# Kernel tuning notes

Measured on AMD Instinct MI355X. Metric: run time of the kernel, lower is better.

The kernel has to match this reference:

```python
import jax, jax.numpy as jnp
import numpy as np

NUM_EMBEDDINGS = 1024
EMBEDDING_DIM = 64
COMMITMENT_COST = 0.25
EPS = 1e-12  # F.normalize clamp eps


def _l2_normalize(v):
    n = jnp.linalg.norm(v, axis=-1, keepdims=True)
    return v / jnp.maximum(n, EPS)


def setup_inputs() -> dict:
    key = jax.random.key(0)
    k_x, k_w = jax.random.split(key)
    x = jax.random.normal(k_x, (262144, EMBEDDING_DIM), dtype=jnp.float32)
    # nn.init.uniform_(weight, -1/K, 1/K)
    lim = 1.0 / NUM_EMBEDDINGS
    codebook = jax.random.uniform(k_w, (NUM_EMBEDDINGS, EMBEDDING_DIM),
                                  minval=-lim, maxval=lim, dtype=jnp.float32)
    return {"x": x, "codebook": codebook}


def reference(x, codebook):
    # Normalized vectors used only for nearest-neighbor search.
    xn = _l2_normalize(x)                      # [N, D]
    cn = _l2_normalize(codebook)               # [K, D]
    # ||xn||^2 + ||cn||^2 - 2 xn.cn  -> [N, K]
    distances = (jnp.sum(xn * xn, axis=1, keepdims=True)
                 + jnp.sum(cn * cn, axis=1)
                 - 2.0 * jnp.einsum('nd,kd->nk', xn, cn))
    encoding_indices = jnp.argmin(distances, axis=1)           # [N]
    quantized_unnormalized = codebook[encoding_indices]        # [N, D]
    sg = jax.lax.stop_gradient
    codebook_loss = jnp.mean((quantized_unnormalized - sg(x)) ** 2)
    commitment_loss = jnp.mean((x - sg(quantized_unnormalized)) ** 2)
    quantized_ste = x + sg(quantized_unnormalized - x)
    return quantized_ste, codebook_loss, commitment_loss, encoding_indices
```

## Files before the change

### kernel.cpp

```cpp
#include <hip/hip_runtime.h>
#include <math.h>

#define EPS 1e-12f
constexpr int N_ROWS = 262144;
constexpr int KCODES = 1024;
constexpr int DIM    = 64;
constexpr int CAP    = 65536;
constexpr int CHUNK_SH = 16384;

typedef __attribute__((ext_vector_type(8)))  short  short8;
typedef __attribute__((ext_vector_type(16))) float  float16;

__device__ inline unsigned short f2bf(float f) {
    unsigned int u = __float_as_uint(f);
    u = u + 0x7fff + ((u >> 16) & 1);
    return (unsigned short)(u >> 16);
}
__device__ inline float bf2f(unsigned short s) {
    return __uint_as_float(((unsigned int)s) << 16);
}

__global__ __launch_bounds__(64)
void vq_prep(const float* __restrict__ cb, float* __restrict__ cnT,
             float* __restrict__ cc, unsigned short* __restrict__ frag,
             int* __restrict__ cnt, float* __restrict__ dloss) {
    int n = blockIdx.x;
    int d = threadIdx.x;
    float v = cb[n * DIM + d];
    float s = v * v;
    #pragma unroll
    for (int off = 32; off; off >>= 1) s += __shfl_xor(s, off, 64);
    float vn = v / fmaxf(sqrtf(s), EPS);
    cnT[d * KCODES + n] = vn;
    float s2 = vn * vn;
    #pragma unroll
    for (int off = 32; off; off >>= 1) s2 += __shfl_xor(s2, off, 64);
    if (d == 0) cc[n] = s2;
    unsigned short hi = f2bf(vn);
    unsigned short lo = f2bf(vn - bf2f(hi));
    int c = n >> 7, t = (n >> 5) & 3;
    int lane = (n & 31) + 32 * ((d >> 3) & 1);
    int si = d >> 4, j = d & 7;
    size_t base = (size_t)(((c * 4 + t) * 4 + si) * 2) * 512 + lane * 8 + j;
    frag[base]       = hi;
    frag[base + 512] = lo;
    if (n == 0 && d == 0) { *cnt = 0; *dloss = 0.f; }
}

__global__ __launch_bounds__(256, 2)
void vq_mfma(const float* __restrict__ x, const unsigned short* __restrict__ frag,
             const float* __restrict__ cb, float* __restrict__ out_q,
             float* __restrict__ out_idx, int* __restrict__ cnt,
             int* __restrict__ list, float* __restrict__ partial) {
    __shared__ unsigned short Blds[2][CHUNK_SH];
    __shared__ int   ridx[256];
    __shared__ float redl[4];

    const int tid = threadIdx.x;
    const int w = tid >> 6, l = tid & 63;
    const int lc = l & 31, h = l >> 5;
    const int row0 = blockIdx.x * 256;

    short8 ahi[2][4], alo[2][4];
    #pragma unroll
    for (int tile = 0; tile < 2; ++tile) {
        int row = row0 + w * 64 + tile * 32 + lc;
        float xv[4][8]; float ss = 0.f;
        #pragma unroll
        for (int s = 0; s < 4; ++s) {
            const float* p = x + (size_t)row * DIM + s * 16 + h * 8;
            float4 a = *(const float4*)p;
            float4 b = *(const float4*)(p + 4);
            xv[s][0]=a.x; xv[s][1]=a.y; xv[s][2]=a.z; xv[s][3]=a.w;
            xv[s][4]=b.x; xv[s][5]=b.y; xv[s][6]=b.z; xv[s][7]=b.w;
            ss += a.x*a.x + a.y*a.y + a.z*a.z + a.w*a.w
                + b.x*b.x + b.y*b.y + b.z*b.z + b.w*b.w;
        }
        ss += __shfl_xor(ss, 32, 64);
        float inv = 1.0f / fmaxf(sqrtf(ss), EPS);
        #pragma unroll
        for (int s = 0; s < 4; ++s)
            #pragma unroll
            for (int j = 0; j < 8; ++j) {
                float v = xv[s][j] * inv;
                unsigned short hb = f2bf(v);
                unsigned short lb = f2bf(v - bf2f(hb));
                ahi[tile][s][j] = (short)hb;
                alo[tile][s][j] = (short)lb;
            }
    }

    int m1[2][16], m2[2][16];
    #pragma unroll
    for (int tile = 0; tile < 2; ++tile)
        #pragma unroll
        for (int r = 0; r < 16; ++r) { m1[tile][r] = 0; m2[tile][r] = 0; }

    {
        const unsigned short* g = frag + (w * 8) * 512 + l * 8;
        #pragma unroll
        for (int q = 0; q < 8; ++q)
            __builtin_amdgcn_global_load_lds(
                (const __attribute__((address_space(1))) unsigned int*)(g + q * 512),
                (__attribute__((address_space(3))) unsigned int*)&Blds[0][(w * 8 + q) * 512],
                16, 0, 0);
    }

    for (int c = 0; c < 8; ++c) {
        __syncthreads();
        if (c < 7) {
            const unsigned short* g = frag + (size_t)(c + 1) * CHUNK_SH + (w * 8) * 512 + l * 8;
            #pragma unroll
            for (int q = 0; q < 8; ++q)
                __builtin_amdgcn_global_load_lds(
                    (const __attribute__((address_space(1))) unsigned int*)(g + q * 512),
                    (__attribute__((address_space(3))) unsigned int*)&Blds[(c + 1) & 1][(w * 8 + q) * 512],
                    16, 0, 0);
        }
        const unsigned short* B = Blds[c & 1];
        #pragma unroll
        for (int t = 0; t < 4; ++t) {
            short8 bhi[4], blo[4];
            #pragma unroll
            for (int s = 0; s < 4; ++s) {
                bhi[s] = *((const short8*)&B[((t * 4 + s) * 2    ) * 512] + l);
                blo[s] = *((const short8*)&B[((t * 4 + s) * 2 + 1) * 512] + l);
            }
            int vcode = (1023 - c * 128 - t * 32) - lc;
            #pragma unroll
            for (int tile = 0; tile < 2; ++tile) {
                float16 acc;
                #pragma unroll
                for (int r = 0; r < 16; ++r) acc[r] = 2.0f;
                #pragma unroll
                for (int s = 0; s < 4; ++s) {
                    acc = __builtin_amdgcn_mfma_f32_32x32x16_bf16(ahi[tile][s], bhi[s], acc, 0, 0, 0);
                    acc = __builtin_amdgcn_mfma_f32_32x32x16_bf16(alo[tile][s], bhi[s], acc, 0, 0, 0);
                    acc = __builtin_amdgcn_mfma_f32_32x32x16_bf16(ahi[tile][s], blo[s], acc, 0, 0, 0);
                }
                #pragma unroll
                for (int r = 0; r < 16; ++r) {
                    int k = (__float_as_int(acc[r]) & (int)0xFFFFFC00) | vcode;
                    int t0 = min(m1[tile][r], k);
                    m1[tile][r] = max(m1[tile][r], k);
                    m2[tile][r] = max(m2[tile][r], t0);
                }
            }
        }
    }

    #pragma unroll
    for (int tile = 0; tile < 2; ++tile)
        #pragma unroll
        for (int r = 0; r < 16; ++r) {
            int a = m1[tile][r], b = m2[tile][r];
            #pragma unroll
            for (int off = 1; off < 32; off <<= 1) {
                int oa = __shfl_xor(a, off, 64);
                int ob = __shfl_xor(b, off, 64);
                int nb = max(max(b, ob), min(a, oa));
                a = max(a, oa); b = nb;
            }
            if (lc == 0) {
                int rowl = w * 64 + tile * 32 + (r & 3) + 8 * (r >> 2) + 4 * h;
                ridx[rowl] = 1023 - (a & 1023);
                if (((a >> 10) - (b >> 10)) <= 1) {
                    int p = atomicAdd(cnt, 1);
                    if (p < CAP) list[p] = row0 + rowl;
                }
            }
        }
    __syncthreads();

    out_idx[row0 + tid] = (float)ridx[tid];

    float lsum = 0.f;
    const float4* cb4 = (const float4*)cb;
    const float4* x4  = (const float4*)x;
    float4*       o4  = (float4*)out_q;
    #pragma unroll
    for (int i = 0; i < 16; ++i) {
        int f = tid + 256 * i;
        int r = f >> 4, c4 = f & 15;
        float4 q  = cb4[ridx[r] * 16 + c4];
        float4 xr = x4[(size_t)row0 * 16 + f];
        o4[(size_t)row0 * 16 + f] = q;
        float dx = q.x - xr.x, dy = q.y - xr.y, dz = q.z - xr.z, dw = q.w - xr.w;
        lsum += dx * dx + dy * dy + dz * dz + dw * dw;
    }
    #pragma unroll
    for (int off = 32; off; off >>= 1) lsum += __shfl_xor(lsum, off, 64);
    if (l == 0) redl[w] = lsum;
    __syncthreads();
    if (tid == 0) partial[blockIdx.x] = redl[0] + redl[1] + redl[2] + redl[3];
}

__global__ __launch_bounds__(256)
void vq_recheck(const float* __restrict__ x, const float* __restrict__ cnT,
                const float* __restrict__ cc, const float* __restrict__ cb,
                const int* __restrict__ cnt, const int* __restrict__ list,
                float* __restrict__ out_idx, float* __restrict__ out_q,
                float* __restrict__ dloss) {
    int w = threadIdx.x >> 6, l = threadIdx.x & 63;
    int wid = blockIdx.x * 4 + w, nw = gridDim.x * 4;
    int n = *cnt; if (n > CAP) n = CAP;
    for (int e = wid; e < n; e += nw) {
        int row = list[e];
        float xl = x[(size_t)row * DIM + l];
        float ss = xl * xl;
        #pragma unroll
        for (int off = 32; off; off >>= 1) ss += __shfl_xor(ss, off, 64);
        float inv = 1.0f / fmaxf(sqrtf(ss), EPS);
        float dot[16];
        #pragma unroll
        for (int kk = 0; kk < 16; ++kk) dot[kk] = 0.f;
        for (int d = 0; d < 64; ++d) {
            float xd = __shfl(xl, d, 64);
            #pragma unroll
            for (int kk = 0; kk < 16; ++kk)
                dot[kk] = fmaf(xd, cnT[d * KCODES + l + 64 * kk], dot[kk]);
        }
        float best = INFINITY; int bix = 0x7fffffff;
        #pragma unroll
        for (int kk = 0; kk < 16; ++kk) {
            int k = l + 64 * kk;
            float dist = cc[k] - 2.0f * (inv * dot[kk]);
            if (dist < best) { best = dist; bix = k; }
        }
        #pragma unroll
        for (int off = 1; off < 64; off <<= 1) {
            float ob = __shfl_xor(best, off, 64);
            int   oi = __shfl_xor(bix,  off, 64);
            if (ob < best || (ob == best && oi < bix)) { best = ob; bix = oi; }
        }
        int oldi = (int)out_idx[row];
        if (bix != oldi) {
            float qn = cb[(size_t)bix  * DIM + l];
            float qo = cb[(size_t)oldi * DIM + l];
            float an = qn - xl, ao = qo - xl;
            float dl = an * an - ao * ao;
            #pragma unroll
            for (int off = 32; off; off >>= 1) dl += __shfl_xor(dl, off, 64);
            out_q[(size_t)row * DIM + l] = qn;
            if (l == 0) { out_idx[row] = (float)bix; atomicAdd(dloss, dl); }
        }
    }
}

__global__ __launch_bounds__(256)
void vq_final(const float* __restrict__ partial, const float* __restrict__ dloss,
              float* __restrict__ out_loss) {
    float s = 0.f;
    for (int i = threadIdx.x; i < 1024; i += 256) s += partial[i];
    #pragma unroll
    for (int off = 32; off; off >>= 1) s += __shfl_xor(s, off, 64);
    __shared__ float red[4];
    if ((threadIdx.x & 63) == 0) red[threadIdx.x >> 6] = s;
    __syncthreads();
    if (threadIdx.x == 0) {
        float t = red[0] + red[1] + red[2] + red[3] + *dloss;
        float m = t / (float)((size_t)N_ROWS * DIM);
        out_loss[0] = m;
        out_loss[1] = m;
    }
}

extern "C" void kernel_launch(void* const* d_in, const int* in_sizes, int n_in,
                              void* d_out, int out_size, void* d_ws, size_t ws_size,
                              hipStream_t stream) {
    const float* x  = (const float*)d_in[0];
    const float* cb = (const float*)d_in[1];
    float* out = (float*)d_out;
    float* out_q    = out;
    float* out_loss = out + (size_t)N_ROWS * DIM;
    float* out_idx  = out_loss + 2;

    char* ws = (char*)d_ws;
    float*          cnT     = (float*)(ws);
    float*          cc      = (float*)(ws + 262144);
    unsigned short* frag    = (unsigned short*)(ws + 266240);
    int*            cnt     = (int*)(ws + 528384);
    float*          dloss   = (float*)(ws + 528388);
    int*            list    = (int*)(ws + 528400);
    float*          partial = (float*)(ws + 790544);

    vq_prep   <<<KCODES, 64, 0, stream>>>(cb, cnT, cc, frag, cnt, dloss);
    vq_mfma   <<<N_ROWS / 256, 256, 0, stream>>>(x, frag, cb, out_q, out_idx, cnt, list, partial);
    vq_recheck<<<512, 256, 0, stream>>>(x, cnT, cc, cb, cnt, list, out_idx, out_q, dloss);
    vq_final  <<<1, 256, 0, stream>>>(partial, dloss, out_loss);
}
```

Measured before the change: 240.3 us.

## Halve rows per block and codebook chunk to raise occupancy, batch recheck atomics

The main MFMA kernel now processes 128 rows per block with one 32-row tile per wave instead of two, halving A-fragment and min-tracking registers and raising the launch-bounds occupancy target from 2 to 4 blocks. The codebook LDS chunk is halved to 64 codes, with the prep kernel's fragment layout changed to match and 16 pipeline iterations instead of 8. Near-tie rows flagged for the exact recheck are now collected per wave with one batched atomicAdd instead of one atomic per row. The cost is that each codebook B fragment read from LDS is reused by one tile instead of two, more blocks load the full codebook, and there are twice as many partial sums.

New measurement: 246.4 us. 1.03x slower.

```diff
diff --git a/kernel.cpp b/kernel.cpp
--- a/kernel.cpp
+++ b/kernel.cpp
@@ -6,7 +6,7 @@
 constexpr int KCODES = 1024;
 constexpr int DIM    = 64;
 constexpr int CAP    = 65536;
-constexpr int CHUNK_SH = 16384;
+constexpr int CHUNK_SH = 8192;
 
 typedef __attribute__((ext_vector_type(8)))  short  short8;
 typedef __attribute__((ext_vector_type(16))) float  float16;
@@ -20,12 +20,12 @@
     return __uint_as_float(((unsigned int)s) << 16);
 }
 
-__global__ __launch_bounds__(64)
+__global__ __launch_bounds__(256)
 void vq_prep(const float* __restrict__ cb, float* __restrict__ cnT,
              float* __restrict__ cc, unsigned short* __restrict__ frag,
              int* __restrict__ cnt, float* __restrict__ dloss) {
-    int n = blockIdx.x;
-    int d = threadIdx.x;
+    int n = blockIdx.x * 4 + (threadIdx.x >> 6);
+    int d = threadIdx.x & 63;
     float v = cb[n * DIM + d];
     float s = v * v;
     #pragma unroll
@@ -38,33 +38,32 @@
     if (d == 0) cc[n] = s2;
     unsigned short hi = f2bf(vn);
     unsigned short lo = f2bf(vn - bf2f(hi));
-    int c = n >> 7, t = (n >> 5) & 3;
+    int c = n >> 6, t = (n >> 5) & 1;
     int lane = (n & 31) + 32 * ((d >> 3) & 1);
     int si = d >> 4, j = d & 7;
-    size_t base = (size_t)(((c * 4 + t) * 4 + si) * 2) * 512 + lane * 8 + j;
+    size_t base = (size_t)c * CHUNK_SH + (size_t)((t * 4 + si) * 2) * 512 + lane * 8 + j;
     frag[base]       = hi;
     frag[base + 512] = lo;
     if (n == 0 && d == 0) { *cnt = 0; *dloss = 0.f; }
 }
 
-__global__ __launch_bounds__(256, 2)
+__global__ __launch_bounds__(256, 4)
 void vq_mfma(const float* __restrict__ x, const unsigned short* __restrict__ frag,
              const float* __restrict__ cb, float* __restrict__ out_q,
              float* __restrict__ out_idx, int* __restrict__ cnt,
              int* __restrict__ list, float* __restrict__ partial) {
     __shared__ unsigned short Blds[2][CHUNK_SH];
-    __shared__ int   ridx[256];
+    __shared__ int   ridx[128];
     __shared__ float redl[4];
 
     const int tid = threadIdx.x;
     const int w = tid >> 6, l = tid & 63;
     const int lc = l & 31, h = l >> 5;
-    const int row0 = blockIdx.x * 256;
-
-    short8 ahi[2][4], alo[2][4];
-    #pragma unroll
-    for (int tile = 0; tile < 2; ++tile) {
-        int row = row0 + w * 64 + tile * 32 + lc;
+    const int row0 = blockIdx.x * 128;
+    const int row  = row0 + w * 32 + lc;
+
+    short8 ahi[4], alo[4];
+    {
         float xv[4][8]; float ss = 0.f;
         #pragma unroll
         for (int s = 0; s < 4; ++s) {
@@ -85,101 +84,107 @@
                 float v = xv[s][j] * inv;
                 unsigned short hb = f2bf(v);
                 unsigned short lb = f2bf(v - bf2f(hb));
-                ahi[tile][s][j] = (short)hb;
-                alo[tile][s][j] = (short)lb;
-            }
-    }
-
-    int m1[2][16], m2[2][16];
-    #pragma unroll
-    for (int tile = 0; tile < 2; ++tile)
-        #pragma unroll
-        for (int r = 0; r < 16; ++r) { m1[tile][r] = 0; m2[tile][r] = 0; }
+                ahi[s][j] = (short)hb;
+                alo[s][j] = (short)lb;
+            }
+    }
+
+    int m1[16], m2[16];
+    #pragma unroll
+    for (int r = 0; r < 16; ++r) { m1[r] = 0; m2[r] = 0; }
 
     {
-        const unsigned short* g = frag + (w * 8) * 512 + l * 8;
-        #pragma unroll
-        for (int q = 0; q < 8; ++q)
+        const unsigned short* g = frag + tid * 8;
+        #pragma unroll
+        for (int q = 0; q < 4; ++q)
             __builtin_amdgcn_global_load_lds(
-                (const __attribute__((address_space(1))) unsigned int*)(g + q * 512),
-                (__attribute__((address_space(3))) unsigned int*)&Blds[0][(w * 8 + q) * 512],
+                (const __attribute__((address_space(1))) unsigned int*)(g + q * 2048),
+                (__attribute__((address_space(3))) unsigned int*)&Blds[0][(tid + 256 * q) * 8],
                 16, 0, 0);
     }
 
-    for (int c = 0; c < 8; ++c) {
+    for (int c = 0; c < 16; ++c) {
         __syncthreads();
-        if (c < 7) {
-            const unsigned short* g = frag + (size_t)(c + 1) * CHUNK_SH + (w * 8) * 512 + l * 8;
-            #pragma unroll
-            for (int q = 0; q < 8; ++q)
+        if (c < 15) {
+            const unsigned short* g = frag + (size_t)(c + 1) * CHUNK_SH + tid * 8;
+            #pragma unroll
+            for (int q = 0; q < 4; ++q)
                 __builtin_amdgcn_global_load_lds(
-                    (const __attribute__((address_space(1))) unsigned int*)(g + q * 512),
-                    (__attribute__((address_space(3))) unsigned int*)&Blds[(c + 1) & 1][(w * 8 + q) * 512],
+                    (const __attribute__((address_space(1))) unsigned int*)(g + q * 2048),
+                    (__attribute__((address_space(3))) unsigned int*)&Blds[(c + 1) & 1][(tid + 256 * q) * 8],
                     16, 0, 0);
         }
         const unsigned short* B = Blds[c & 1];
         #pragma unroll
-        for (int t = 0; t < 4; ++t) {
-            short8 bhi[4], blo[4];
+        for (int t = 0; t < 2; ++t) {
+            float16 acc;
+            #pragma unroll
+            for (int r = 0; r < 16; ++r) acc[r] = 2.0f;
             #pragma unroll
             for (int s = 0; s < 4; ++s) {
-                bhi[s] = *((const short8*)&B[((t * 4 + s) * 2    ) * 512] + l);
-                blo[s] = *((const short8*)&B[((t * 4 + s) * 2 + 1) * 512] + l);
-            }
-            int vcode = (1023 - c * 128 - t * 32) - lc;
-            #pragma unroll
-            for (int tile = 0; tile < 2; ++tile) {
-                float16 acc;
-                #pragma unroll
-                for (int r = 0; r < 16; ++r) acc[r] = 2.0f;
-                #pragma unroll
-                for (int s = 0; s < 4; ++s) {
-                    acc = __builtin_amdgcn_mfma_f32_32x32x16_bf16(ahi[tile][s], bhi[s], acc, 0, 0, 0);
-                    acc = __builtin_amdgcn_mfma_f32_32x32x16_bf16(alo[tile][s], bhi[s], acc, 0, 0, 0);
-                    acc = __builtin_amdgcn_mfma_f32_32x32x16_bf16(ahi[tile][s], blo[s], acc, 0, 0, 0);
-                }
-                #pragma unroll
-                for (int r = 0; r < 16; ++r) {
-                    int k = (__float_as_int(acc[r]) & (int)0xFFFFFC00) | vcode;
-                    int t0 = min(m1[tile][r], k);
-                    m1[tile][r] = max(m1[tile][r], k);
-                    m2[tile][r] = max(m2[tile][r], t0);
-                }
-            }
-        }
-    }
-
-    #pragma unroll
-    for (int tile = 0; tile < 2; ++tile)
-        #pragma unroll
-        for (int r = 0; r < 16; ++r) {
-            int a = m1[tile][r], b = m2[tile][r];
-            #pragma unroll
-            for (int off = 1; off < 32; off <<= 1) {
-                int oa = __shfl_xor(a, off, 64);
-                int ob = __shfl_xor(b, off, 64);
-                int nb = max(max(b, ob), min(a, oa));
-                a = max(a, oa); b = nb;
-            }
-            if (lc == 0) {
-                int rowl = w * 64 + tile * 32 + (r & 3) + 8 * (r >> 2) + 4 * h;
-                ridx[rowl] = 1023 - (a & 1023);
-                if (((a >> 10) - (b >> 10)) <= 1) {
-                    int p = atomicAdd(cnt, 1);
-                    if (p < CAP) list[p] = row0 + rowl;
-                }
-            }
-        }
+                short8 bhi = *((const short8*)&B[((t * 4 + s) * 2    ) * 512] + l);
+                short8 blo = *((const short8*)&B[((t * 4 + s) * 2 + 1) * 512] + l);
+                acc = __builtin_amdgcn_mfma_f32_32x32x16_bf16(ahi[s], bhi, acc, 0, 0, 0);
+                acc = __builtin_amdgcn_mfma_f32_32x32x16_bf16(alo[s], bhi, acc, 0, 0, 0);
+                acc = __builtin_amdgcn_mfma_f32_32x32x16_bf16(ahi[s], blo, acc, 0, 0, 0);
+            }
+            int vcode = (1023 - c * 64 - t * 32) - lc;
+            #pragma unroll
+            for (int r = 0; r < 16; ++r) {
+                int k = (__float_as_int(acc[r]) & (int)0xFFFFFC00) | vcode;
+                int t0 = min(m1[r], k);
+                m1[r] = max(m1[r], k);
+                m2[r] = max(m2[r], t0);
+            }
+        }
+    }
+
+    int flags = 0;
+    #pragma unroll
+    for (int r = 0; r < 16; ++r) {
+        int a = m1[r], b = m2[r];
+        #pragma unroll
+        for (int off = 1; off < 32; off <<= 1) {
+            int oa = __shfl_xor(a, off, 64);
+            int ob = __shfl_xor(b, off, 64);
+            int nb = max(max(b, ob), min(a, oa));
+            a = max(a, oa); b = nb;
+        }
+        if (lc == 0) {
+            int rr = (r & 3) + 8 * (r >> 2) + 4 * h;
+            ridx[w * 32 + rr] = 1023 - (a & 1023);
+            if (((a >> 10) - (b >> 10)) <= 1) flags |= (1 << r);
+        }
+    }
+
+    {
+        int f0 = __shfl(flags, 0, 64), fh = __shfl(flags, 32, 64);
+        int tot = __popc(f0) + __popc(fh);
+        int base = 0;
+        if (l == 0 && tot) base = atomicAdd(cnt, tot);
+        base = __shfl(base, 0, 64);
+        if (tot && (l == 0 || l == 32)) {
+            int off = (l == 32) ? __popc(f0) : 0;
+            int fl = flags;
+            while (fl) {
+                int r = __ffs(fl) - 1; fl &= fl - 1;
+                int rr = (r & 3) + 8 * (r >> 2) + 4 * h;
+                int p = base + off;
+                if (p < CAP) list[p] = row0 + w * 32 + rr;
+                ++off;
+            }
+        }
+    }
     __syncthreads();
 
-    out_idx[row0 + tid] = (float)ridx[tid];
+    if (tid < 128) out_idx[row0 + tid] = (float)ridx[tid];
 
     float lsum = 0.f;
     const float4* cb4 = (const float4*)cb;
     const float4* x4  = (const float4*)x;
     float4*       o4  = (float4*)out_q;
     #pragma unroll
-    for (int i = 0; i < 16; ++i) {
+    for (int i = 0; i < 8; ++i) {
         int f = tid + 256 * i;
         int r = f >> 4, c4 = f & 15;
         float4 q  = cb4[ridx[r] * 16 + c4];
@@ -251,7 +256,7 @@
 void vq_final(const float* __restrict__ partial, const float* __restrict__ dloss,
               float* __restrict__ out_loss) {
     float s = 0.f;
-    for (int i = threadIdx.x; i < 1024; i += 256) s += partial[i];
+    for (int i = threadIdx.x; i < 2048; i += 256) s += partial[i];
     #pragma unroll
     for (int off = 32; off; off >>= 1) s += __shfl_xor(s, off, 64);
     __shared__ float red[4];
@@ -284,8 +289,8 @@
     int*            list    = (int*)(ws + 528400);
     float*          partial = (float*)(ws + 790544);
 
-    vq_prep   <<<KCODES, 64, 0, stream>>>(cb, cnT, cc, frag, cnt, dloss);
-    vq_mfma   <<<N_ROWS / 256, 256, 0, stream>>>(x, frag, cb, out_q, out_idx, cnt, list, partial);
+    vq_prep   <<<KCODES / 4, 256, 0, stream>>>(cb, cnT, cc, frag, cnt, dloss);
+    vq_mfma   <<<N_ROWS / 128, 256, 0, stream>>>(x, frag, cb, out_q, out_idx, cnt, list, partial);
     vq_recheck<<<512, 256, 0, stream>>>(x, cnT, cc, cb, cnt, list, out_idx, out_q, dloss);
     vq_final  <<<1, 256, 0, stream>>>(partial, dloss, out_loss);
 }
```
